# Kernel optimization log

Hardware: AMD Instinct MI355X
Metric: run time of the kernel (lower is better)

Reference implementation:

```python
import jax, jax.numpy as jnp
import numpy as np

OUTPUT_BIT = 8
N_SCALE = 28          # scale_bits
EXP_BITS = 16
SEGMENTS = 16
DEGREE = 2
S_VAL = 0.03          # input quantization scale


def _fit_pieces(s):
    # Mirrors _compute_integer_coefficients for backend='float':
    # fit exp((x_off-127)*s) over offset domain x_off*s in [-128s, 127s].
    xs_off = np.linspace(-128.0, 127.0, 10000)
    ys = np.exp((xs_off - 127.0) * s)
    xs = xs_off * s
    bounds = np.linspace(-128.0 * s, 127.0 * s, SEGMENTS + 1)
    coeffs = np.zeros((SEGMENTS, DEGREE + 1))  # ascending powers a0,a1,a2
    for j in range(SEGMENTS):
        m = (xs >= bounds[j]) & (xs <= bounds[j + 1])
        coeffs[j] = np.polyfit(xs[m], ys[m], DEGREE)[::-1]
    # integer coefficients: p(x_int*s)*2^N = sum_k floor(a_k*s^k*2^N)*x_int^k
    pw = s ** np.arange(DEGREE + 1)
    coeffs_int = np.floor(coeffs * pw[None, :] * (2.0 ** N_SCALE))
    lo_int = np.floor(bounds[:-1] / s)  # integer segment lower bounds
    return lo_int.astype(np.float32), coeffs_int.astype(np.float32)


def setup_inputs() -> dict:
    key = jax.random.key(0)
    x = jax.random.normal(key, (8, 12, 512, 512), dtype=jnp.float32) * 4.0
    scaling_factor = jnp.full((1,), S_VAL, dtype=jnp.float32)
    lo_np, cf_np = _fit_pieces(S_VAL)
    return {
        "x": x,
        "scaling_factor": scaling_factor,
        "lo_bounds": jnp.asarray(lo_np),
        "coeffs": jnp.asarray(cf_np),
    }


def floor_ste(y):
    # floor with straight-through gradient
    return y + jax.lax.stop_gradient(jnp.floor(y) - y)


def reference(x, scaling_factor, lo_bounds, coeffs):
    s = scaling_factor
    x_int = floor_ste(x / s)
    x_int = x_int - jnp.max(x_int, axis=-1, keepdims=True) + 127.0

    # piecewise-polynomial integer exp (computed under no_grad in the original)
    xi = jax.lax.stop_gradient(x_int)
    idx = jnp.clip(jnp.searchsorted(lo_bounds, xi, side="right") - 1, 0, SEGMENTS - 1)
    c = coeffs[idx]                         # [..., deg+1], ascending powers
    r = c[..., DEGREE]
    for k in range(DEGREE - 1, -1, -1):     # Horner evaluation
        r = r * xi + c[..., k]
    exp_int = jnp.maximum(jax.lax.stop_gradient(r), 0.0)

    exp_int = floor_ste(exp_int / 2.0 ** (30 - EXP_BITS + 1))
    exp_sum = jnp.maximum(jnp.sum(exp_int, axis=-1, keepdims=True), 1.0)
    factor = jnp.floor(2.0 ** 32 / jax.lax.stop_gradient(exp_sum))
    softmax_int = jnp.floor(jax.lax.stop_gradient(exp_int) * factor / 2.0 ** (32 - OUTPUT_BIT + 1))

    softmax_float = jax.nn.softmax(x, axis=-1)
    s_out = jnp.array([2.0 / 2 ** OUTPUT_BIT], dtype=x.dtype)
    smi_f = softmax_int * s_out
    # STE: integer value forward, float-softmax gradient backward
    output = jax.lax.stop_gradient(smi_f) + (softmax_float - jax.lax.stop_gradient(softmax_float))
    output = s_out * floor_ste(output / s_out)
    return output, s_out
```

## Files before the change

kernel.cpp:

```cpp
#include <hip/hip_runtime.h>


#define ROWLEN 512

typedef float nfloat4 __attribute__((ext_vector_type(4)));

#define DPP_SUM_I32(t)                                                        \
    t += __builtin_amdgcn_update_dpp(0, t, 0x111, 0xf, 0xf, true);            \
    t += __builtin_amdgcn_update_dpp(0, t, 0x112, 0xf, 0xf, true);            \
    t += __builtin_amdgcn_update_dpp(0, t, 0x114, 0xf, 0xf, true);            \
    t += __builtin_amdgcn_update_dpp(0, t, 0x118, 0xf, 0xf, true);            \
    t += __builtin_amdgcn_update_dpp(0, t, 0x142, 0xa, 0xf, true);            \
    t += __builtin_amdgcn_update_dpp(0, t, 0x143, 0xc, 0xf, true);

#define DPP_MAX_F32_STEP(m, ctrl, rmask)                                      \
    {                                                                         \
        int _mi = __float_as_int(m);                                          \
        int _sh = __builtin_amdgcn_update_dpp(_mi, _mi, ctrl, rmask, 0xf, false); \
        m = fmaxf(m, __int_as_float(_sh));                                    \
    }
#define DPP_MIN_F32_STEP(m, ctrl, rmask)                                      \
    {                                                                         \
        int _mi = __float_as_int(m);                                          \
        int _sh = __builtin_amdgcn_update_dpp(_mi, _mi, ctrl, rmask, 0xf, false); \
        m = fminf(m, __int_as_float(_sh));                                    \
    }

__global__ __launch_bounds__(256, 8) void ppis_kernel(
    const float* __restrict__ x,
    const float* __restrict__ sfp,
    const float* __restrict__ lo,
    const float* __restrict__ cf,
    float* __restrict__ out,
    int nrows)
{
    __shared__ int  s_e[1024];
    __shared__ int4 s_cf[16];

    const int tid  = threadIdx.x;
    const int lane = tid & 63;
    const int wid  = tid >> 6;

    const long long row = (long long)blockIdx.x * 4 + wid;
    const float4* xp = reinterpret_cast<const float4*>(x) + row * (ROWLEN / 4);
    const float4 va = xp[lane];
    const float4 vb = xp[lane + 64];

    const float s  = sfp[0];
    const float ry = 1.0f / s;

    if (tid < 16)
        s_cf[tid] = make_int4((int)cf[tid*3+0], (int)cf[tid*3+1], (int)cf[tid*3+2], 0);

    {
        int4 ev;
        int* evp = reinterpret_cast<int*>(&ev);
        const int j0 = tid * 4;
        #pragma unroll
        for (int jj = 0; jj < 4; ++jj) {
            const int j  = j0 + jj;
            const int u  = j - 768;
            const int uc = u < 0 ? 0 : u;
            int idx = ((uc + 1) * 257) >> 12;
            idx = idx > 15 ? 15 : idx;
            const int c0 = (int)cf[idx * 3 + 0];
            const int c1 = (int)cf[idx * 3 + 1];
            const int c2 = (int)cf[idx * 3 + 2];
            const int xi = j - 896;
            const int r1 = c2 * xi + c1;
            long long r2 = (long long)r1 * xi + c0;
            if (r2 < 0) r2 = 0;
            evp[jj] = (int)(r2 >> 15);
        }
        reinterpret_cast<int4*>(s_e)[tid] = ev;
    }
    __syncthreads();

    const float xv[8] = {va.x, va.y, va.z, va.w, vb.x, vb.y, vb.z, vb.w};

    float mf = fmaxf(fmaxf(fmaxf(xv[0], xv[1]), fmaxf(xv[2], xv[3])),
                     fmaxf(fmaxf(xv[4], xv[5]), fmaxf(xv[6], xv[7])));
    float nf_ = fminf(fminf(fminf(xv[0], xv[1]), fminf(xv[2], xv[3])),
                      fminf(fminf(xv[4], xv[5]), fminf(xv[6], xv[7])));
    DPP_MAX_F32_STEP(mf, 0x111, 0xf)  DPP_MIN_F32_STEP(nf_, 0x111, 0xf)
    DPP_MAX_F32_STEP(mf, 0x112, 0xf)  DPP_MIN_F32_STEP(nf_, 0x112, 0xf)
    DPP_MAX_F32_STEP(mf, 0x114, 0xf)  DPP_MIN_F32_STEP(nf_, 0x114, 0xf)
    DPP_MAX_F32_STEP(mf, 0x118, 0xf)  DPP_MIN_F32_STEP(nf_, 0x118, 0xf)
    DPP_MAX_F32_STEP(mf, 0x142, 0xa)  DPP_MIN_F32_STEP(nf_, 0x142, 0xa)
    DPP_MAX_F32_STEP(mf, 0x143, 0xc)  DPP_MIN_F32_STEP(nf_, 0x143, 0xc)
    const float xmax = __int_as_float(__builtin_amdgcn_readlane(__float_as_int(mf), 63));
    const float xmin = __int_as_float(__builtin_amdgcn_readlane(__float_as_int(nf_), 63));

    auto fdiv_floor = [&](float xk) -> int {
        float nf = floorf(xk * ry);
        const float d = fmaf(-s, nf, xk);
        nf = (d < 0.0f) ? nf - 1.0f : nf;
        const float u = fmaf(-s, nf + 1.0f, xk);
        nf = (u >= 0.0f) ? nf + 1.0f : nf;
        return (int)nf;
    };

    int n[8];
    #pragma unroll
    for (int k = 0; k < 8; ++k) n[k] = fdiv_floor(xv[k]);
    const int mx = fdiv_floor(xmax);
    const int mn = fdiv_floor(xmin);

    const int joff = 1023 - mx;

    int e[8];
    int tsum = 0;
    if (mn + joff >= 0) {
        #pragma unroll
        for (int k = 0; k < 8; ++k) {
            e[k] = s_e[n[k] + joff];
            tsum += e[k];
        }
    } else {
        #pragma unroll
        for (int k = 0; k < 8; ++k) {
            const int u  = n[k] + (255 - mx);
            const int uc = u < 0 ? 0 : u;
            int idx = ((uc + 1) * 257) >> 12;
            idx = idx > 15 ? 15 : idx;
            const int4 c = s_cf[idx];
            const long long xi = (long long)(u - 128);
            long long r2 = ((long long)c.z * xi + c.y) * xi + c.x;
            if (r2 < 0) r2 = 0;
            e[k] = (int)(r2 >> 15);
            tsum += e[k];
        }
    }

    DPP_SUM_I32(tsum)
    int ts = __builtin_amdgcn_readlane(tsum, 63);
    if (ts < 1) ts = 1;

    const unsigned int factor =
        (unsigned int)floor(__ddiv_rn(4294967296.0, (double)ts));

    nfloat4 o0, o1;
    #pragma unroll
    for (int k = 0; k < 4; ++k) {
        const unsigned long long p0 = (unsigned long long)(unsigned int)e[k]   * factor;
        const unsigned long long p1 = (unsigned long long)(unsigned int)e[k+4] * factor;
        o0[k] = (float)(int)(p0 >> 25) * 0.0078125f;
        o1[k] = (float)(int)(p1 >> 25) * 0.0078125f;
    }

    nfloat4* op = reinterpret_cast<nfloat4*>(out) + row * (ROWLEN / 4);
    __builtin_nontemporal_store(o0, op + lane);
    __builtin_nontemporal_store(o1, op + lane + 64);

    if (row == 0 && lane == 0)
        out[(long long)nrows * ROWLEN] = 0.0078125f;
}

extern "C" void kernel_launch(void* const* d_in, const int* in_sizes, int n_in,
                              void* d_out, int out_size, void* d_ws, size_t ws_size,
                              hipStream_t stream) {
    const float* x  = (const float*)d_in[0];
    const float* sf = (const float*)d_in[1];
    const float* lo = (const float*)d_in[2];
    const float* cf = (const float*)d_in[3];
    float* out = (float*)d_out;

    const int nrows = in_sizes[0] / ROWLEN;
    ppis_kernel<<<nrows / 4, 256, 0, stream>>>(x, sf, lo, cf, out, nrows);
}
```

Before: 181.6 us.

## Process two rows per wavefront to amortize LDS exp table build

Each wavefront now handles two softmax rows instead of one, halving the grid so the per-block 1024-entry exp lookup table construction and barrier are amortized over twice as many rows. Row min is shared across both rows for the fast-path check, and exp values are re-read from LDS in the output loop rather than held in registers. The slow path now reads coefficients from global memory instead of a shared int4 table. Occupancy hint drops from 8 to 6 blocks per CU because register pressure rises.

```diff
diff --git a/kernel.cpp b/kernel.cpp
--- a/kernel.cpp
+++ b/kernel.cpp
@@ -26,7 +26,7 @@
         m = fminf(m, __int_as_float(_sh));                                    \
     }
 
-__global__ __launch_bounds__(256, 8) void ppis_kernel(
+__global__ __launch_bounds__(256, 6) void ppis_kernel(
     const float* __restrict__ x,
     const float* __restrict__ sfp,
     const float* __restrict__ lo,
@@ -34,23 +34,22 @@
     float* __restrict__ out,
     int nrows)
 {
-    __shared__ int  s_e[1024];
-    __shared__ int4 s_cf[16];
+    __shared__ int s_e[1024];
 
     const int tid  = threadIdx.x;
     const int lane = tid & 63;
     const int wid  = tid >> 6;
 
-    const long long row = (long long)blockIdx.x * 4 + wid;
-    const float4* xp = reinterpret_cast<const float4*>(x) + row * (ROWLEN / 4);
-    const float4 va = xp[lane];
-    const float4 vb = xp[lane + 64];
+    const long long rowA = ((long long)blockIdx.x * 4 + wid) * 2;
+    const float4* xpA = reinterpret_cast<const float4*>(x) + rowA * (ROWLEN / 4);
+    const float4* xpB = xpA + (ROWLEN / 4);
+    const float4 vaA = xpA[lane];
+    const float4 vbA = xpA[lane + 64];
+    const float4 vaB = xpB[lane];
+    const float4 vbB = xpB[lane + 64];
 
     const float s  = sfp[0];
     const float ry = 1.0f / s;
-
-    if (tid < 16)
-        s_cf[tid] = make_int4((int)cf[tid*3+0], (int)cf[tid*3+1], (int)cf[tid*3+2], 0);
 
     {
         int4 ev;
@@ -76,20 +75,27 @@
     }
     __syncthreads();
 
-    const float xv[8] = {va.x, va.y, va.z, va.w, vb.x, vb.y, vb.z, vb.w};
+    const float xvA[8] = {vaA.x, vaA.y, vaA.z, vaA.w, vbA.x, vbA.y, vbA.z, vbA.w};
+    const float xvB[8] = {vaB.x, vaB.y, vaB.z, vaB.w, vbB.x, vbB.y, vbB.z, vbB.w};
 
-    float mf = fmaxf(fmaxf(fmaxf(xv[0], xv[1]), fmaxf(xv[2], xv[3])),
-                     fmaxf(fmaxf(xv[4], xv[5]), fmaxf(xv[6], xv[7])));
-    float nf_ = fminf(fminf(fminf(xv[0], xv[1]), fminf(xv[2], xv[3])),
-                      fminf(fminf(xv[4], xv[5]), fminf(xv[6], xv[7])));
-    DPP_MAX_F32_STEP(mf, 0x111, 0xf)  DPP_MIN_F32_STEP(nf_, 0x111, 0xf)
-    DPP_MAX_F32_STEP(mf, 0x112, 0xf)  DPP_MIN_F32_STEP(nf_, 0x112, 0xf)
-    DPP_MAX_F32_STEP(mf, 0x114, 0xf)  DPP_MIN_F32_STEP(nf_, 0x114, 0xf)
-    DPP_MAX_F32_STEP(mf, 0x118, 0xf)  DPP_MIN_F32_STEP(nf_, 0x118, 0xf)
-    DPP_MAX_F32_STEP(mf, 0x142, 0xa)  DPP_MIN_F32_STEP(nf_, 0x142, 0xa)
-    DPP_MAX_F32_STEP(mf, 0x143, 0xc)  DPP_MIN_F32_STEP(nf_, 0x143, 0xc)
-    const float xmax = __int_as_float(__builtin_amdgcn_readlane(__float_as_int(mf), 63));
-    const float xmin = __int_as_float(__builtin_amdgcn_readlane(__float_as_int(nf_), 63));
+    float mfA = fmaxf(fmaxf(fmaxf(xvA[0], xvA[1]), fmaxf(xvA[2], xvA[3])),
+                      fmaxf(fmaxf(xvA[4], xvA[5]), fmaxf(xvA[6], xvA[7])));
+    float mfB = fmaxf(fmaxf(fmaxf(xvB[0], xvB[1]), fmaxf(xvB[2], xvB[3])),
+                      fmaxf(fmaxf(xvB[4], xvB[5]), fmaxf(xvB[6], xvB[7])));
+    float mng = fminf(
+        fminf(fminf(fminf(xvA[0], xvA[1]), fminf(xvA[2], xvA[3])),
+              fminf(fminf(xvA[4], xvA[5]), fminf(xvA[6], xvA[7]))),
+        fminf(fminf(fminf(xvB[0], xvB[1]), fminf(xvB[2], xvB[3])),
+              fminf(fminf(xvB[4], xvB[5]), fminf(xvB[6], xvB[7]))));
+    DPP_MAX_F32_STEP(mfA, 0x111, 0xf) DPP_MAX_F32_STEP(mfB, 0x111, 0xf) DPP_MIN_F32_STEP(mng, 0x111, 0xf)
+    DPP_MAX_F32_STEP(mfA, 0x112, 0xf) DPP_MAX_F32_STEP(mfB, 0x112, 0xf) DPP_MIN_F32_STEP(mng, 0x112, 0xf)
+    DPP_MAX_F32_STEP(mfA, 0x114, 0xf) DPP_MAX_F32_STEP(mfB, 0x114, 0xf) DPP_MIN_F32_STEP(mng, 0x114, 0xf)
+    DPP_MAX_F32_STEP(mfA, 0x118, 0xf) DPP_MAX_F32_STEP(mfB, 0x118, 0xf) DPP_MIN_F32_STEP(mng, 0x118, 0xf)
+    DPP_MAX_F32_STEP(mfA, 0x142, 0xa) DPP_MAX_F32_STEP(mfB, 0x142, 0xa) DPP_MIN_F32_STEP(mng, 0x142, 0xa)
+    DPP_MAX_F32_STEP(mfA, 0x143, 0xc) DPP_MAX_F32_STEP(mfB, 0x143, 0xc) DPP_MIN_F32_STEP(mng, 0x143, 0xc)
+    const float xmaxA = __int_as_float(__builtin_amdgcn_readlane(__float_as_int(mfA), 63));
+    const float xmaxB = __int_as_float(__builtin_amdgcn_readlane(__float_as_int(mfB), 63));
+    const float xming = __int_as_float(__builtin_amdgcn_readlane(__float_as_int(mng), 63));
 
     auto fdiv_floor = [&](float xk) -> int {
         float nf = floorf(xk * ry);
@@ -100,59 +106,80 @@
         return (int)nf;
     };
 
-    int n[8];
+    int nA[8], nB[8];
     #pragma unroll
-    for (int k = 0; k < 8; ++k) n[k] = fdiv_floor(xv[k]);
-    const int mx = fdiv_floor(xmax);
-    const int mn = fdiv_floor(xmin);
+    for (int k = 0; k < 8; ++k) { nA[k] = fdiv_floor(xvA[k]); nB[k] = fdiv_floor(xvB[k]); }
+    const int mxA = fdiv_floor(xmaxA);
+    const int mxB = fdiv_floor(xmaxB);
+    const int mng_i = fdiv_floor(xming);
 
-    const int joff = 1023 - mx;
+    const int joffA = 1023 - mxA;
+    const int joffB = 1023 - mxB;
 
-    int e[8];
-    int tsum = 0;
-    if (mn + joff >= 0) {
+    auto eval_exact = [&](int nk, int mx) -> int {
+        const int u  = nk - mx + 255;
+        const int uc = u < 0 ? 0 : u;
+        int idx = ((uc + 1) * 257) >> 12;
+        idx = idx > 15 ? 15 : idx;
+        const long long c0 = (long long)cf[idx * 3 + 0];
+        const long long c1 = (long long)cf[idx * 3 + 1];
+        const long long c2 = (long long)cf[idx * 3 + 2];
+        const long long xi = (long long)(u - 128);
+        long long r2 = (c2 * xi + c1) * xi + c0;
+        if (r2 < 0) r2 = 0;
+        return (int)(r2 >> 15);
+    };
+
+    const bool fast = (mng_i + joffA >= 0) && (mng_i + joffB >= 0);
+
+    int tsA = 0, tsB = 0;
+    if (fast) {
         #pragma unroll
         for (int k = 0; k < 8; ++k) {
-            e[k] = s_e[n[k] + joff];
-            tsum += e[k];
+            tsA += s_e[nA[k] + joffA];
+            tsB += s_e[nB[k] + joffB];
         }
     } else {
         #pragma unroll
         for (int k = 0; k < 8; ++k) {
-            const int u  = n[k] + (255 - mx);
-            const int uc = u < 0 ? 0 : u;
-            int idx = ((uc + 1) * 257) >> 12;
-            idx = idx > 15 ? 15 : idx;
-            const int4 c = s_cf[idx];
-            const long long xi = (long long)(u - 128);
-            long long r2 = ((long long)c.z * xi + c.y) * xi + c.x;
-            if (r2 < 0) r2 = 0;
-            e[k] = (int)(r2 >> 15);
-            tsum += e[k];
+            tsA += eval_exact(nA[k], mxA);
+            tsB += eval_exact(nB[k], mxB);
         }
     }
 
-    DPP_SUM_I32(tsum)
-    int ts = __builtin_amdgcn_readlane(tsum, 63);
-    if (ts < 1) ts = 1;
+    DPP_SUM_I32(tsA)
+    DPP_SUM_I32(tsB)
+    int sA = __builtin_amdgcn_readlane(tsA, 63);
+    int sB = __builtin_amdgcn_readlane(tsB, 63);
+    if (sA < 1) sA = 1;
+    if (sB < 1) sB = 1;
 
-    const unsigned int factor =
-        (unsigned int)floor(__ddiv_rn(4294967296.0, (double)ts));
+    const unsigned int factorA =
+        (unsigned int)floor(__ddiv_rn(4294967296.0, (double)sA));
+    const unsigned int factorB =
+        (unsigned int)floor(__ddiv_rn(4294967296.0, (double)sB));
 
-    nfloat4 o0, o1;
+    nfloat4 oA0, oA1, oB0, oB1;
     #pragma unroll
     for (int k = 0; k < 4; ++k) {
-        const unsigned long long p0 = (unsigned long long)(unsigned int)e[k]   * factor;
-        const unsigned long long p1 = (unsigned long long)(unsigned int)e[k+4] * factor;
-        o0[k] = (float)(int)(p0 >> 25) * 0.0078125f;
-        o1[k] = (float)(int)(p1 >> 25) * 0.0078125f;
+        const unsigned int eA0 = fast ? (unsigned int)s_e[nA[k]   + joffA] : (unsigned int)eval_exact(nA[k],   mxA);
+        const unsigned int eA1 = fast ? (unsigned int)s_e[nA[k+4] + joffA] : (unsigned int)eval_exact(nA[k+4], mxA);
+        const unsigned int eB0 = fast ? (unsigned int)s_e[nB[k]   + joffB] : (unsigned int)eval_exact(nB[k],   mxB);
+        const unsigned int eB1 = fast ? (unsigned int)s_e[nB[k+4] + joffB] : (unsigned int)eval_exact(nB[k+4], mxB);
+        oA0[k] = (float)(int)(((unsigned long long)eA0 * factorA) >> 25) * 0.0078125f;
+        oA1[k] = (float)(int)(((unsigned long long)eA1 * factorA) >> 25) * 0.0078125f;
+        oB0[k] = (float)(int)(((unsigned long long)eB0 * factorB) >> 25) * 0.0078125f;
+        oB1[k] = (float)(int)(((unsigned long long)eB1 * factorB) >> 25) * 0.0078125f;
     }
 
-    nfloat4* op = reinterpret_cast<nfloat4*>(out) + row * (ROWLEN / 4);
-    __builtin_nontemporal_store(o0, op + lane);
-    __builtin_nontemporal_store(o1, op + lane + 64);
+    nfloat4* opA = reinterpret_cast<nfloat4*>(out) + rowA * (ROWLEN / 4);
+    nfloat4* opB = opA + (ROWLEN / 4);
+    __builtin_nontemporal_store(oA0, opA + lane);
+    __builtin_nontemporal_store(oA1, opA + lane + 64);
+    __builtin_nontemporal_store(oB0, opB + lane);
+    __builtin_nontemporal_store(oB1, opB + lane + 64);
 
-    if (row == 0 && lane == 0)
+    if (rowA == 0 && lane == 0)
         out[(long long)nrows * ROWLEN] = 0.0078125f;
 }
 
@@ -166,5 +193,5 @@
     float* out = (float*)d_out;
 
     const int nrows = in_sizes[0] / ROWLEN;
-    ppis_kernel<<<nrows / 4, 256, 0, stream>>>(x, sf, lo, cf, out, nrows);
+    ppis_kernel<<<nrows / 8, 256, 0, stream>>>(x, sf, lo, cf, out, nrows);
 }
```

Result: slower. 186.1 us (+2.5%).
